# Kernel optimization log

Measured on AMD Instinct MI355X. Metric: run time of the kernel, lower is better.

Reference implementation:

```python
import jax, jax.numpy as jnp
import numpy as np

N_NODES = 4096
D_MODEL = 1024
MAX_DEPS = 8
N_CLASSES = 64


def setup_inputs() -> dict:
    key = jax.random.key(0)
    k1, k2, k3 = jax.random.split(key, 3)
    questions = jax.random.normal(k1, (N_NODES, D_MODEL), dtype=jnp.float32)
    # Padded dependency lists; every dependency index is strictly < node index,
    # so processing nodes in index order is a valid topological order.
    rng = np.random.default_rng(0)
    dep_idx = np.zeros((N_NODES, MAX_DEPS), dtype=np.int32)
    dep_mask = np.zeros((N_NODES, MAX_DEPS), dtype=np.int32)
    for i in range(1, N_NODES):
        nd = int(rng.integers(1, MAX_DEPS + 1))
        dep_idx[i, :nd] = rng.integers(0, i, size=nd)
        dep_mask[i, :nd] = 1
    W1 = jax.random.normal(k2, (D_MODEL, 2 * D_MODEL), dtype=jnp.float32) * 0.02
    b1 = jnp.zeros((D_MODEL,), dtype=jnp.float32)
    W2 = jax.random.normal(k3, (N_CLASSES, D_MODEL), dtype=jnp.float32) * 0.02
    b2 = jnp.zeros((N_CLASSES,), dtype=jnp.float32)
    return {
        "questions": questions,
        "W1": W1,
        "b1": b1,
        "W2": W2,
        "b2": b2,
        "dep_idx": jnp.asarray(dep_idx),
        "dep_mask": jnp.asarray(dep_mask),
    }


def reference(questions, W1, b1, W2, b2, dep_idx, dep_mask):
    n_nodes, d_model = questions.shape

    def step(answers, xs):
        i, q, deps, mask = xs
        ctx = answers[deps]                       # [MAX_DEPS, d_model] gather
        m = mask.astype(q.dtype)
        # masked mean; all-zero mask -> zero context (matches torch zeros branch)
        ctx_mean = (ctx * m[:, None]).sum(0) / jnp.maximum(m.sum(), 1.0)
        combined = jnp.concatenate([q, ctx_mean])  # [2*d_model]
        h = jax.nn.gelu(combined @ W1.T + b1, approximate=False)
        return answers.at[i].set(h), None

    answers0 = jnp.zeros((n_nodes, d_model), dtype=questions.dtype)
    xs = (jnp.arange(n_nodes), questions, dep_idx, dep_mask)
    answers, _ = jax.lax.scan(step, answers0, xs)
    root_answer = answers[n_nodes - 1]            # root = last node in topo order
    return root_answer @ W2.T + b2                # [n_classes] logits
```

## Files before the change

### kernel.cpp

```cpp
#include <hip/hip_runtime.h>

#define NN 4096
#define DM 1024
#define MD 8
#define NW 256
#define NCOL 4
#define NT 512
#define NWAVE (NT / 64)
#define UR 4
#define MAXL 4097

#define MI_NLEV 0
#define MI_ROOTPOS 1
#define MI_ARRIVE 8
#define MI_LO 1024
#define MI_NL 6144
#define MI_PERM 10240
#define MI_DCNT 14336
#define MI_INV 18432
#define MI_DPOS 22528

typedef __attribute__((ext_vector_type(8))) short bf16x8;
typedef __attribute__((ext_vector_type(8))) unsigned short ushort8;
typedef __attribute__((ext_vector_type(4))) float f32x4;

__device__ __forceinline__ float gelu_f(float x) {
  return 0.5f * x * (1.0f + erff(x * 0.70710678118654752440f));
}
__device__ __forceinline__ unsigned short f2bf(float x) {
  unsigned int u = __builtin_bit_cast(unsigned int, x);
  u += 0x7FFFu + ((u >> 16) & 1u);
  return (unsigned short)(u >> 16);
}
__device__ __forceinline__ float bf2f(unsigned short v) {
  return __builtin_bit_cast(float, (unsigned int)v << 16);
}

__global__ __launch_bounds__(1024) void k_cvt(
    const float* __restrict__ Q, unsigned short* __restrict__ Qb) {
  const int t = threadIdx.x;
  const size_t total = (size_t)NN * DM / 8;
  for (size_t c = (size_t)blockIdx.x * 1024 + t; c < total; c += 255 * 1024) {
    const size_t i = c * 8;
    float4 a = *(const float4*)&Q[i];
    float4 b = *(const float4*)&Q[i + 4];
    ushort8 o;
    o[0] = f2bf(a.x); o[1] = f2bf(a.y); o[2] = f2bf(a.z); o[3] = f2bf(a.w);
    o[4] = f2bf(b.x); o[5] = f2bf(b.y); o[6] = f2bf(b.z); o[7] = f2bf(b.w);
    *(ushort8*)&Qb[i] = o;
  }
}

__global__ __launch_bounds__(1024) void k_fused(
    const unsigned short* __restrict__ Qb, const float* __restrict__ W1,
    const float* __restrict__ b1, const int* __restrict__ dep_idx,
    const int* __restrict__ dep_mask, int* __restrict__ meta,
    float* __restrict__ preQ) {
  __shared__ int lvl[NN];
  __shared__ int liv[NN];
  __shared__ int cnt[2 * NN];
  __shared__ int pos[NN];
  __shared__ int s_changed, s_max;
  const int t = threadIdx.x;

  if (blockIdx.x != 0) {
    if (t >= 256) return;
    const int bid = blockIdx.x - 1;
    const int wave = t >> 6, lane = t & 63;
    const int wm = wave >> 1, wn = wave & 1;
    const int m0 = (bid >> 3) * 128 + wm * 64;
    const int n0 = (bid & 7) * 128 + wn * 64;
    const int lrow = lane & 15;
    const int klo = (lane >> 4) * 8;
    f32x4 acc[4][4] = {};
    for (int k0 = 0; k0 < DM; k0 += 32) {
      bf16x8 af[4];
      #pragma unroll
      for (int f = 0; f < 4; ++f)
        af[f] = *(const bf16x8*)&Qb[(size_t)(m0 + f * 16 + lrow) * DM + k0 + klo];
      bf16x8 bfr[4];
      #pragma unroll
      for (int g = 0; g < 4; ++g) {
        const float* wsrc = &W1[(size_t)(n0 + g * 16 + lrow) * 2048 + k0 + klo];
        float4 w0 = *(const float4*)&wsrc[0];
        float4 w1 = *(const float4*)&wsrc[4];
        bf16x8 bb;
        bb[0] = (short)f2bf(w0.x); bb[1] = (short)f2bf(w0.y);
        bb[2] = (short)f2bf(w0.z); bb[3] = (short)f2bf(w0.w);
        bb[4] = (short)f2bf(w1.x); bb[5] = (short)f2bf(w1.y);
        bb[6] = (short)f2bf(w1.z); bb[7] = (short)f2bf(w1.w);
        bfr[g] = bb;
      }
      #pragma unroll
      for (int f = 0; f < 4; ++f)
        #pragma unroll
        for (int g = 0; g < 4; ++g)
          acc[f][g] = __builtin_amdgcn_mfma_f32_16x16x32_bf16(af[f], bfr[g], acc[f][g], 0, 0, 0);
    }
    float b1v[4];
    #pragma unroll
    for (int g = 0; g < 4; ++g) b1v[g] = b1[n0 + g * 16 + lrow];
    const int mrow = (lane >> 4) * 4;
    #pragma unroll
    for (int f = 0; f < 4; ++f)
      #pragma unroll
      for (int g = 0; g < 4; ++g) {
        const int n = n0 + g * 16 + lrow;
        #pragma unroll
        for (int r = 0; r < 4; ++r)
          preQ[(size_t)(m0 + f * 16 + mrow + r) * DM + n] = acc[f][g][r] + b1v[g];
      }
    return;
  }

  for (int i = t; i < NN; i += 1024) { lvl[i] = 0; liv[i] = (i == NN - 1) ? 1 : 0; }
  for (int i = t; i < 2 * NN; i += 1024) cnt[i] = 0;
  if (t == 0) s_max = 0;
  __syncthreads();

  for (int u = 0; u < 4; ++u) {
    const int i = u * 1024 + t;
    const int4 d0 = *(const int4*)&dep_idx[i * MD];
    const int4 d1 = *(const int4*)&dep_idx[i * MD + 4];
    const int4 m0 = *(const int4*)&dep_mask[i * MD];
    const int4 m1 = *(const int4*)&dep_mask[i * MD + 4];
    int my = 0;
    for (;;) {
      if (t == 0) s_changed = 0;
      __syncthreads();
      int m = 0;
      if (m0.x) { int l = lvl[d0.x] + 1; m = m > l ? m : l; }
      if (m0.y) { int l = lvl[d0.y] + 1; m = m > l ? m : l; }
      if (m0.z) { int l = lvl[d0.z] + 1; m = m > l ? m : l; }
      if (m0.w) { int l = lvl[d0.w] + 1; m = m > l ? m : l; }
      if (m1.x) { int l = lvl[d1.x] + 1; m = m > l ? m : l; }
      if (m1.y) { int l = lvl[d1.y] + 1; m = m > l ? m : l; }
      if (m1.z) { int l = lvl[d1.z] + 1; m = m > l ? m : l; }
      if (m1.w) { int l = lvl[d1.w] + 1; m = m > l ? m : l; }
      if (m > my) { my = m; lvl[i] = m; s_changed = 1; }
      __syncthreads();
      if (!s_changed) break;
    }
  }
  for (int u = 3; u >= 0; --u) {
    const int i = u * 1024 + t;
    const int4 d0 = *(const int4*)&dep_idx[i * MD];
    const int4 d1 = *(const int4*)&dep_idx[i * MD + 4];
    const int4 m0 = *(const int4*)&dep_mask[i * MD];
    const int4 m1 = *(const int4*)&dep_mask[i * MD + 4];
    for (;;) {
      if (t == 0) s_changed = 0;
      __syncthreads();
      bool ch = false;
      if (liv[i]) {
        if (m0.x && !liv[d0.x]) { liv[d0.x] = 1; ch = true; }
        if (m0.y && !liv[d0.y]) { liv[d0.y] = 1; ch = true; }
        if (m0.z && !liv[d0.z]) { liv[d0.z] = 1; ch = true; }
        if (m0.w && !liv[d0.w]) { liv[d0.w] = 1; ch = true; }
        if (m1.x && !liv[d1.x]) { liv[d1.x] = 1; ch = true; }
        if (m1.y && !liv[d1.y]) { liv[d1.y] = 1; ch = true; }
        if (m1.z && !liv[d1.z]) { liv[d1.z] = 1; ch = true; }
        if (m1.w && !liv[d1.w]) { liv[d1.w] = 1; ch = true; }
      }
      if (ch) s_changed = 1;
      __syncthreads();
      if (!s_changed) break;
    }
  }
  for (int i = t; i < NN; i += 1024) {
    atomicAdd(&cnt[2 * lvl[i] + (liv[i] ? 0 : 1)], 1);
    atomicMax(&s_max, lvl[i]);
  }
  __syncthreads();
  const int nL = s_max + 1;
  if (t == 0) {
    int off = 0;
    for (int l = 0; l < nL; ++l) {
      meta[MI_LO + l] = off;
      meta[MI_NL + l] = cnt[2 * l];
      const int a = cnt[2 * l], b = cnt[2 * l + 1];
      cnt[2 * l] = off; off += a;
      cnt[2 * l + 1] = off; off += b;
    }
    meta[MI_LO + nL] = off;
    meta[MI_NLEV] = nL;
  }
  __syncthreads();
  for (int i = t; i < NN; i += 1024)
    pos[i] = atomicAdd(&cnt[2 * lvl[i] + (liv[i] ? 0 : 1)], 1);
  __syncthreads();
  for (int i = t; i < NN; i += 1024) {
    const int r = pos[i];
    meta[MI_PERM + r] = i;
    const int4 d0 = *(const int4*)&dep_idx[i * MD];
    const int4 d1 = *(const int4*)&dep_idx[i * MD + 4];
    const int4 m0 = *(const int4*)&dep_mask[i * MD];
    const int4 m1 = *(const int4*)&dep_mask[i * MD + 4];
    const int dd[8] = {d0.x, d0.y, d0.z, d0.w, d1.x, d1.y, d1.z, d1.w};
    const int mm[8] = {m0.x, m0.y, m0.z, m0.w, m1.x, m1.y, m1.z, m1.w};
    int nd = 0;
    #pragma unroll
    for (int k = 0; k < MD; ++k)
      if (mm[k]) { meta[MI_DPOS + r * MD + nd] = pos[dd[k]]; ++nd; }
    for (int k = nd; k < MD; ++k) meta[MI_DPOS + r * MD + k] = 0;
    meta[MI_DCNT + r] = nd;
    ((float*)meta)[MI_INV + r] = nd ? 1.0f / (float)nd : 0.0f;
  }
  if (t == 0) meta[MI_ROOTPOS] = pos[NN - 1];
  for (int i = t; i < NW; i += 1024) meta[MI_ARRIVE + i] = 0;
}

__global__ __launch_bounds__(NT) void k_levels(
    const float* __restrict__ W1, const float* __restrict__ preQ,
    unsigned short* __restrict__ hPb, float4* __restrict__ gPan, int* __restrict__ meta,
    const float* __restrict__ W2, const float* __restrict__ b2, float* __restrict__ out) {
  const int tid = threadIdx.x;
  const int wb = blockIdx.x;
  const int c0 = wb * NCOL;
  const int wave = tid >> 6, lane = tid & 63;
  const int nL = meta[MI_NLEV];
  const int rootRow = meta[MI_ROOTPOS];
  __shared__ int s_lo[MAXL];
  __shared__ int s_nl[MAXL];
  __shared__ float4 preLDS[NT];
  for (int i = tid; i <= nL; i += NT) s_lo[i] = meta[MI_LO + i];
  for (int i = tid; i < nL; i += NT) s_nl[i] = meta[MI_NL + i];
  float4 wreg[NCOL][4];
  #pragma unroll
  for (int cc = 0; cc < NCOL; ++cc)
    #pragma unroll
    for (int q = 0; q < 4; ++q)
      wreg[cc][q] = *(const float4*)&W1[(size_t)(c0 + cc) * 2048 + 1024 + lane * 16 + q * 4];
  __syncthreads();
  float4* gp = gPan + (size_t)wb * NN;
  const float* invA = (const float*)&meta[MI_INV];

  for (int l = 0; l < nL; ++l) {
    const int lo = s_lo[l];
    const int nA = s_nl[l];

    for (int r = lo + tid; r < lo + nA; r += NT) {
      const int node = meta[MI_PERM + r];
      const int nd = meta[MI_DCNT + r];
      const float iv = invA[r];
      const int4 p0 = *(const int4*)&meta[MI_DPOS + r * MD];
      const int4 p1 = *(const int4*)&meta[MI_DPOS + r * MD + 4];
      const int dps[8] = {p0.x, p0.y, p0.z, p0.w, p1.x, p1.y, p1.z, p1.w};
      float sx = 0.f, sy = 0.f, sz = 0.f, sw = 0.f;
      #pragma unroll
      for (int d = 0; d < MD; ++d) {
        float4 v = gp[dps[d]];
        sx += (d < nd) ? v.x : 0.f;
        sy += (d < nd) ? v.y : 0.f;
        sz += (d < nd) ? v.z : 0.f;
        sw += (d < nd) ? v.w : 0.f;
      }
      const float4 pq = (l > 0 && r == lo + tid) ? preLDS[tid]
                                                 : *(const float4*)&preQ[(size_t)node * DM + c0];
      const unsigned short h0 = f2bf(gelu_f(pq.x + sx * iv));
      const unsigned short h1 = f2bf(gelu_f(pq.y + sy * iv));
      const unsigned short h2 = f2bf(gelu_f(pq.z + sz * iv));
      const unsigned short h3 = f2bf(gelu_f(pq.w + sw * iv));
      const unsigned long long u = (unsigned long long)h0 | ((unsigned long long)h1 << 16)
                                 | ((unsigned long long)h2 << 32) | ((unsigned long long)h3 << 48);
      __hip_atomic_store((unsigned long long*)&hPb[(size_t)r * DM + c0], u,
                         __ATOMIC_RELAXED, __HIP_MEMORY_SCOPE_AGENT);
    }
    __syncthreads();
    if (tid == 0)
      __hip_atomic_store(&meta[MI_ARRIVE + wb], l + 1, __ATOMIC_RELAXED, __HIP_MEMORY_SCOPE_AGENT);
    if (l + 1 < nL && tid < s_nl[l + 1]) {
      const int node2 = meta[MI_PERM + s_lo[l + 1] + tid];
      preLDS[tid] = *(const float4*)&preQ[(size_t)node2 * DM + c0];
    }
    if (tid < 64) {
      for (;;) {
        int m = 1 << 30;
        #pragma unroll
        for (int u = 0; u < 4; ++u) {
          int v = __hip_atomic_load(&meta[MI_ARRIVE + tid * 4 + u], __ATOMIC_RELAXED, __HIP_MEMORY_SCOPE_AGENT);
          m = v < m ? v : m;
        }
        #pragma unroll
        for (int off = 1; off < 64; off <<= 1) {
          int o = __shfl_xor(m, off);
          m = o < m ? o : m;
        }
        if (m >= l + 1) break;
        __builtin_amdgcn_s_sleep(1);
      }
    }
    __syncthreads();

    for (int base = wave * UR; base < nA; base += NWAVE * UR) {
      const int cnt = nA - base;
      ushort8 hv[UR][2];
      #pragma unroll
      for (int u = 0; u < UR; ++u) {
        const int r = lo + base + ((u < cnt) ? u : 0);
        const ushort8* h8 = (const ushort8*)&hPb[(size_t)r * DM];
        hv[u][0] = h8[lane * 2];
        hv[u][1] = h8[lane * 2 + 1];
      }
      float rr[UR][NCOL];
      #pragma unroll
      for (int u = 0; u < UR; ++u) {
        float hf[16];
        #pragma unroll
        for (int e = 0; e < 8; ++e) { hf[e] = bf2f(hv[u][0][e]); hf[8 + e] = bf2f(hv[u][1][e]); }
        #pragma unroll
        for (int cc = 0; cc < NCOL; ++cc) {
          float a = 0.f;
          #pragma unroll
          for (int q = 0; q < 4; ++q)
            a += hf[q * 4 + 0] * wreg[cc][q].x + hf[q * 4 + 1] * wreg[cc][q].y
               + hf[q * 4 + 2] * wreg[cc][q].z + hf[q * 4 + 3] * wreg[cc][q].w;
          rr[u][cc] = a;
        }
      }
      #pragma unroll
      for (int off = 1; off < 64; off <<= 1)
        #pragma unroll
        for (int u = 0; u < UR; ++u)
          #pragma unroll
          for (int cc = 0; cc < NCOL; ++cc)
            rr[u][cc] += __shfl_xor(rr[u][cc], off);
      if (lane == 0) {
        #pragma unroll
        for (int u = 0; u < UR; ++u)
          if (u < cnt) gp[lo + base + u] = make_float4(rr[u][0], rr[u][1], rr[u][2], rr[u][3]);
      }
    }
    __syncthreads();
  }

  if (wb == 0) {
    float* red = (float*)preLDS;
    const int j = tid >> 3, kc = tid & 7;
    const ushort8* h8 = (const ushort8*)&hPb[(size_t)rootRow * DM];
    const float* wr2 = W2 + (size_t)j * DM;
    float acc = 0.f;
    for (int k = kc * 128; k < kc * 128 + 128; k += 8) {
      ushort8 hv = h8[k >> 3];
      float4 wa = *(const float4*)&wr2[k];
      float4 wb4 = *(const float4*)&wr2[k + 4];
      acc += bf2f(hv[0]) * wa.x + bf2f(hv[1]) * wa.y + bf2f(hv[2]) * wa.z + bf2f(hv[3]) * wa.w
           + bf2f(hv[4]) * wb4.x + bf2f(hv[5]) * wb4.y + bf2f(hv[6]) * wb4.z + bf2f(hv[7]) * wb4.w;
    }
    red[tid] = acc;
    __syncthreads();
    if (kc == 0) {
      float s = 0.f;
      #pragma unroll
      for (int e = 0; e < 8; ++e) s += red[j * 8 + e];
      out[j] = s + b2[j];
    }
  }
}

extern "C" void kernel_launch(void* const* d_in, const int* in_sizes, int n_in,
                              void* d_out, int out_size, void* d_ws, size_t ws_size,
                              hipStream_t stream) {
  const float* Q        = (const float*)d_in[0];
  const float* W1       = (const float*)d_in[1];
  const float* b1       = (const float*)d_in[2];
  const float* W2       = (const float*)d_in[3];
  const float* b2       = (const float*)d_in[4];
  const int*   dep_idx  = (const int*)d_in[5];
  const int*   dep_mask = (const int*)d_in[6];

  char* ws = (char*)d_ws;
  float*          preQ = (float*)ws;
  unsigned short* hPb  = (unsigned short*)(ws + (16ull << 20));
  unsigned short* Qb   = (unsigned short*)(ws + (24ull << 20));
  float4*         gPan = (float4*)(ws + (32ull << 20));
  int*            meta = (int*)(ws + (48ull << 20));
  float*          out  = (float*)d_out;

  k_cvt<<<dim3(255), dim3(1024), 0, stream>>>(Q, Qb);
  k_fused<<<dim3(257), dim3(1024), 0, stream>>>(Qb, W1, b1, dep_idx, dep_mask, meta, preQ);
  k_levels<<<dim3(NW), dim3(NT), 0, stream>>>(W1, preQ, hPb, gPan, meta, W2, b2, out);
}
```

Measured before the change: 482.5 us.

## Halve persistent workgroups to 128, each owning eight output columns

After: 876.8 us. 1.82x slower.

```diff
diff --git a/kernel.cpp b/kernel.cpp
--- a/kernel.cpp
+++ b/kernel.cpp
@@ -3,8 +3,8 @@
 #define NN 4096
 #define DM 1024
 #define MD 8
-#define NW 256
-#define NCOL 4
+#define NW 128
+#define NCOL 8
 #define NT 512
 #define NWAVE (NT / 64)
 #define UR 4
@@ -222,7 +222,7 @@
   const int rootRow = meta[MI_ROOTPOS];
   __shared__ int s_lo[MAXL];
   __shared__ int s_nl[MAXL];
-  __shared__ float4 preLDS[NT];
+  __shared__ float4 preLDS[NT][2];
   for (int i = tid; i <= nL; i += NT) s_lo[i] = meta[MI_LO + i];
   for (int i = tid; i < nL; i += NT) s_nl[i] = meta[MI_NL + i];
   float4 wreg[NCOL][4];
@@ -232,7 +232,7 @@
     for (int q = 0; q < 4; ++q)
       wreg[cc][q] = *(const float4*)&W1[(size_t)(c0 + cc) * 2048 + 1024 + lane * 16 + q * 4];
   __syncthreads();
-  float4* gp = gPan + (size_t)wb * NN;
+  float4* gp = gPan + (size_t)wb * NN * 2;
   const float* invA = (const float*)&meta[MI_INV];
 
   for (int l = 0; l < nL; ++l) {
@@ -246,39 +246,49 @@
       const int4 p0 = *(const int4*)&meta[MI_DPOS + r * MD];
       const int4 p1 = *(const int4*)&meta[MI_DPOS + r * MD + 4];
       const int dps[8] = {p0.x, p0.y, p0.z, p0.w, p1.x, p1.y, p1.z, p1.w};
-      float sx = 0.f, sy = 0.f, sz = 0.f, sw = 0.f;
+      float s[8] = {};
       #pragma unroll
       for (int d = 0; d < MD; ++d) {
-        float4 v = gp[dps[d]];
-        sx += (d < nd) ? v.x : 0.f;
-        sy += (d < nd) ? v.y : 0.f;
-        sz += (d < nd) ? v.z : 0.f;
-        sw += (d < nd) ? v.w : 0.f;
-      }
-      const float4 pq = (l > 0 && r == lo + tid) ? preLDS[tid]
-                                                 : *(const float4*)&preQ[(size_t)node * DM + c0];
-      const unsigned short h0 = f2bf(gelu_f(pq.x + sx * iv));
-      const unsigned short h1 = f2bf(gelu_f(pq.y + sy * iv));
-      const unsigned short h2 = f2bf(gelu_f(pq.z + sz * iv));
-      const unsigned short h3 = f2bf(gelu_f(pq.w + sw * iv));
-      const unsigned long long u = (unsigned long long)h0 | ((unsigned long long)h1 << 16)
-                                 | ((unsigned long long)h2 << 32) | ((unsigned long long)h3 << 48);
-      __hip_atomic_store((unsigned long long*)&hPb[(size_t)r * DM + c0], u,
-                         __ATOMIC_RELAXED, __HIP_MEMORY_SCOPE_AGENT);
+        float4 va = gp[2 * dps[d]];
+        float4 vb = gp[2 * dps[d] + 1];
+        const bool ok = (d < nd);
+        s[0] += ok ? va.x : 0.f; s[1] += ok ? va.y : 0.f;
+        s[2] += ok ? va.z : 0.f; s[3] += ok ? va.w : 0.f;
+        s[4] += ok ? vb.x : 0.f; s[5] += ok ? vb.y : 0.f;
+        s[6] += ok ? vb.z : 0.f; s[7] += ok ? vb.w : 0.f;
+      }
+      float4 pqa, pqb;
+      if (l > 0 && r == lo + tid) { pqa = preLDS[tid][0]; pqb = preLDS[tid][1]; }
+      else {
+        pqa = *(const float4*)&preQ[(size_t)node * DM + c0];
+        pqb = *(const float4*)&preQ[(size_t)node * DM + c0 + 4];
+      }
+      const float pq[8] = {pqa.x, pqa.y, pqa.z, pqa.w, pqb.x, pqb.y, pqb.z, pqb.w};
+      unsigned short h[8];
+      #pragma unroll
+      for (int j = 0; j < 8; ++j) h[j] = f2bf(gelu_f(pq[j] + s[j] * iv));
+      const unsigned long long u0 = (unsigned long long)h[0] | ((unsigned long long)h[1] << 16)
+                                  | ((unsigned long long)h[2] << 32) | ((unsigned long long)h[3] << 48);
+      const unsigned long long u1 = (unsigned long long)h[4] | ((unsigned long long)h[5] << 16)
+                                  | ((unsigned long long)h[6] << 32) | ((unsigned long long)h[7] << 48);
+      unsigned long long* hrow = (unsigned long long*)&hPb[(size_t)r * DM + c0];
+      __hip_atomic_store(&hrow[0], u0, __ATOMIC_RELAXED, __HIP_MEMORY_SCOPE_AGENT);
+      __hip_atomic_store(&hrow[1], u1, __ATOMIC_RELAXED, __HIP_MEMORY_SCOPE_AGENT);
     }
     __syncthreads();
     if (tid == 0)
       __hip_atomic_store(&meta[MI_ARRIVE + wb], l + 1, __ATOMIC_RELAXED, __HIP_MEMORY_SCOPE_AGENT);
     if (l + 1 < nL && tid < s_nl[l + 1]) {
       const int node2 = meta[MI_PERM + s_lo[l + 1] + tid];
-      preLDS[tid] = *(const float4*)&preQ[(size_t)node2 * DM + c0];
+      preLDS[tid][0] = *(const float4*)&preQ[(size_t)node2 * DM + c0];
+      preLDS[tid][1] = *(const float4*)&preQ[(size_t)node2 * DM + c0 + 4];
     }
     if (tid < 64) {
       for (;;) {
         int m = 1 << 30;
         #pragma unroll
-        for (int u = 0; u < 4; ++u) {
-          int v = __hip_atomic_load(&meta[MI_ARRIVE + tid * 4 + u], __ATOMIC_RELAXED, __HIP_MEMORY_SCOPE_AGENT);
+        for (int u = 0; u < 2; ++u) {
+          int v = __hip_atomic_load(&meta[MI_ARRIVE + tid * 2 + u], __ATOMIC_RELAXED, __HIP_MEMORY_SCOPE_AGENT);
           m = v < m ? v : m;
         }
         #pragma unroll
@@ -328,7 +338,10 @@
       if (lane == 0) {
         #pragma unroll
         for (int u = 0; u < UR; ++u)
-          if (u < cnt) gp[lo + base + u] = make_float4(rr[u][0], rr[u][1], rr[u][2], rr[u][3]);
+          if (u < cnt) {
+            gp[2 * (lo + base + u)] = make_float4(rr[u][0], rr[u][1], rr[u][2], rr[u][3]);
+            gp[2 * (lo + base + u) + 1] = make_float4(rr[u][4], rr[u][5], rr[u][6], rr[u][7]);
+          }
       }
     }
     __syncthreads();
```
